# Performance work log

Measured on AMD Instinct MI355X. Metric: run time of the kernel, lower is better.

## Reference

```python
import jax, jax.numpy as jnp
import numpy as np

B, S, E, H = 2, 2048, 768, 12
HD = E // H
EPS = 1e-5


def setup_inputs() -> dict:
    key = jax.random.key(0)
    ks = jax.random.split(key, 7)
    sc_in = 1.0 / np.sqrt(E)
    return {
        "x": jax.random.normal(ks[0], (B, S, E), dtype=jnp.float32),
        "gamma": jnp.ones((E,), dtype=jnp.float32),
        "beta": jnp.zeros((E,), dtype=jnp.float32),
        "Wqkv": jax.random.normal(ks[1], (3 * E, E), dtype=jnp.float32) * sc_in,
        "bqkv": jax.random.normal(ks[2], (3 * E,), dtype=jnp.float32) * 0.01,
        "Wo": jax.random.normal(ks[3], (E, E), dtype=jnp.float32) * sc_in,
        "bo": jax.random.normal(ks[4], (E,), dtype=jnp.float32) * 0.01,
    }


def reference(x, gamma, beta, Wqkv, bqkv, Wo, bo):
    # LayerNorm
    mu = jnp.mean(x, axis=-1, keepdims=True)
    var = jnp.mean(jnp.square(x - mu), axis=-1, keepdims=True)
    xn = (x - mu) * jax.lax.rsqrt(var + EPS) * gamma + beta
    # fused QKV projection; original reshapes to [B,S,H,3*hd] then chunks,
    # i.e. per-head blocks of 3*hd split into q/k/v slices of hd each.
    qkv = (xn @ Wqkv.T + bqkv).reshape(B, S, H, 3, HD)
    q, k, v = qkv[..., 0, :], qkv[..., 1, :], qkv[..., 2, :]  # [B,S,H,hd]
    scores = jnp.einsum("bshd,bthd->bhst", q, k) / np.sqrt(HD)
    attn = jax.nn.softmax(scores, axis=-1)  # [B,H,S,S]
    out = jnp.einsum("bhst,bthd->bshd", attn, v).reshape(B, S, E)
    return out @ Wo.T + bo
```

## Files before the change

kernel.cpp:

```cpp
#include <hip/hip_runtime.h>
#include <math.h>

#define B_  2
#define S_  2048
#define E_  768
#define H_  12
#define HD_ 64
#define M_  (B_ * S_)
#define N3E (3 * E_)

typedef __attribute__((ext_vector_type(8)))  short short8;
typedef __attribute__((ext_vector_type(8)))  _Float16 half8;
typedef __attribute__((ext_vector_type(4)))  _Float16 half4;
typedef __attribute__((ext_vector_type(2)))  _Float16 half2_t;
typedef __attribute__((ext_vector_type(4)))  float floatx4;
typedef __attribute__((ext_vector_type(16))) float floatx16;

#define QSCALE 0.18033688011112042f

__device__ inline unsigned short f2bf(float f) {
  union { float f; unsigned u; } a; a.f = f;
  unsigned r = a.u + 0x7fff + ((a.u >> 16) & 1);
  return (unsigned short)(r >> 16);
}
__device__ inline unsigned short f2bf_fast(float f) {
  union { float f; unsigned u; } a; a.f = f;
  return (unsigned short)((a.u + 0x8000u) >> 16);
}
__device__ inline half2_t pkrtz(float a, float b) {
  return __builtin_bit_cast(half2_t, __builtin_amdgcn_cvt_pkrtz(a, b));
}

__global__ __launch_bounds__(256) void cvt_kernel(
    const float* __restrict__ src, unsigned short* __restrict__ dst, int n4) {
  int i = blockIdx.x * 256 + threadIdx.x;
  if (i < n4) {
    float4 f = *(const float4*)&src[i * 4];
    ushort4 r;
    r.x = f2bf(f.x); r.y = f2bf(f.y); r.z = f2bf(f.z); r.w = f2bf(f.w);
    *(ushort4*)&dst[i * 4] = r;
  }
}

__global__ __launch_bounds__(256) void ln_kernel(
    const float* __restrict__ x, const float* __restrict__ gamma,
    const float* __restrict__ beta, unsigned short* __restrict__ xnb) {
  const int row = blockIdx.x;
  const int t = threadIdx.x;
  const float* xr = x + (size_t)row * E_;

  float v0 = xr[t];
  float v1 = xr[t + 256];
  float v2 = xr[t + 512];
  float s  = v0 + v1 + v2;
  float s2 = v0 * v0 + v1 * v1 + v2 * v2;

  for (int o = 32; o > 0; o >>= 1) {
    s  += __shfl_down(s, o);
    s2 += __shfl_down(s2, o);
  }
  __shared__ float red[8];
  const int wave = t >> 6, lane = t & 63;
  if (lane == 0) { red[wave] = s; red[4 + wave] = s2; }
  __syncthreads();
  s  = red[0] + red[1] + red[2] + red[3];
  s2 = red[4] + red[5] + red[6] + red[7];

  const float mu  = s * (1.0f / E_);
  const float var = s2 * (1.0f / E_) - mu * mu;
  const float rs  = rsqrtf(var + 1e-5f);

  unsigned short* xo = xnb + (size_t)row * E_;
  xo[t]       = f2bf((v0 - mu) * rs * gamma[t]       + beta[t]);
  xo[t + 256] = f2bf((v1 - mu) * rs * gamma[t + 256] + beta[t + 256]);
  xo[t + 512] = f2bf((v2 - mu) * rs * gamma[t + 512] + beta[t + 512]);
}

__global__ __launch_bounds__(256) void bgemm_kernel(
    const unsigned short* __restrict__ A, const unsigned short* __restrict__ Wb,
    const float* __restrict__ bias, int mode,
    unsigned short* __restrict__ qbf, unsigned short* __restrict__ kbf,
    _Float16* __restrict__ vth, float* __restrict__ out) {
  __shared__ __align__(16) unsigned short As[128 * 64];
  __shared__ __align__(16) unsigned short Bs[128 * 64];

  const int t  = threadIdx.x;
  const int ln = t & 63, wv = t >> 6;
  const int lr = ln & 15, lg = ln >> 4;
  const int wr = wv >> 1, wc = wv & 1;
  const int m0 = blockIdx.x * 128, n0 = blockIdx.y * 128;

  const int srow = ln >> 3;
  const int scol = (ln & 7) * 8;

  const unsigned short* Ag = A  + (size_t)(m0 + wv * 32 + srow) * 768 + scol;
  const unsigned short* Bg = Wb + (size_t)(n0 + wv * 32 + srow) * 768 + scol;

  floatx4 acc[4][4];
#pragma unroll
  for (int i = 0; i < 4; i++)
#pragma unroll
    for (int j = 0; j < 4; j++) acc[i][j] = (floatx4){0.f, 0.f, 0.f, 0.f};

  for (int k0 = 0; k0 < 768; k0 += 64) {
    __syncthreads();
#pragma unroll
    for (int j = 0; j < 4; j++) {
      __builtin_amdgcn_global_load_lds(
          (const __attribute__((address_space(1))) void*)(Ag + k0 + j * 8 * 768),
          (__attribute__((address_space(3))) void*)(&As[(wv * 32 + j * 8) * 64]),
          16, 0, 0);
      __builtin_amdgcn_global_load_lds(
          (const __attribute__((address_space(1))) void*)(Bg + k0 + j * 8 * 768),
          (__attribute__((address_space(3))) void*)(&Bs[(wv * 32 + j * 8) * 64]),
          16, 0, 0);
    }
    __syncthreads();

#pragma unroll
    for (int kk = 0; kk < 2; kk++) {
      short8 af[4], bf[4];
#pragma unroll
      for (int i = 0; i < 4; i++)
        af[i] = *(const short8*)&As[(wr * 64 + i * 16 + lr) * 64 + kk * 32 + lg * 8];
#pragma unroll
      for (int j = 0; j < 4; j++)
        bf[j] = *(const short8*)&Bs[(wc * 64 + j * 16 + lr) * 64 + kk * 32 + lg * 8];
#pragma unroll
      for (int i = 0; i < 4; i++)
#pragma unroll
        for (int j = 0; j < 4; j++)
          acc[i][j] = __builtin_amdgcn_mfma_f32_16x16x32_bf16(af[i], bf[j], acc[i][j], 0, 0, 0);
    }
  }

  if (mode == 1) {
#pragma unroll
    for (int i = 0; i < 4; i++) {
      const int grow0 = m0 + wr * 64 + i * 16 + lg * 4;
#pragma unroll
      for (int j = 0; j < 4; j++) {
        const int gcol = n0 + wc * 64 + j * 16 + lr;
        const float bb = bias[gcol];
#pragma unroll
        for (int r = 0; r < 4; r++)
          out[(size_t)(grow0 + r) * E_ + gcol] = acc[i][j][r] + bb;
      }
    }
  } else {
#pragma unroll
    for (int i = 0; i < 4; i++) {
      const int grow0 = m0 + wr * 64 + i * 16 + lg * 4;
      const int bq = grow0 >> 11, s0 = grow0 & 2047;
      const int tb = s0 >> 6, kh = (s0 >> 5) & 1;
#pragma unroll
      for (int j = 0; j < 4; j++) {
        const int n = n0 + wc * 64 + j * 16 + lr;
        const int h = n / 192, w = (n >> 6) % 3, d = n & 63;
        const int bh = bq * H_ + h;
        const float bb = bias[n];
        if (w == 2) {
          const int db = d >> 5, l31v = d & 31;
          const int kc2 = (s0 >> 4) & 1, l5v = (s0 >> 3) & 1, e0 = s0 & 7;
          half2_t h01 = pkrtz(acc[i][j][0] + bb, acc[i][j][1] + bb);
          half2_t h23 = pkrtz(acc[i][j][2] + bb, acc[i][j][3] + bb);
          half4 hv = __builtin_shufflevector(h01, h23, 0, 1, 2, 3);
          const size_t idx =
              ((((((size_t)bh * 32 + tb) * 2 + kh) * 2 + db) * 2 + kc2) * 2 + l5v) * 256
              + (size_t)l31v * 8 + e0;
          *(half4*)&vth[idx] = hv;
        } else {
          unsigned short* dst = (w == 0) ? qbf : kbf;
          const float sc = (w == 0) ? QSCALE : 1.0f;
          const int kc = d >> 4, l5 = (d >> 3) & 1, e = d & 7;
          const size_t basei =
              ((((size_t)bh * 32 + tb) * 2 + kh) * 4 + kc) * 512 + (size_t)l5 * 256 + e;
          const int r0 = (s0 & 31) * 8;
#pragma unroll
          for (int r = 0; r < 4; r++)
            dst[basei + r0 + r * 8] = f2bf_fast((acc[i][j][r] + bb) * sc);
        }
      }
    }
  }
}

#define PROW 40

__global__ __launch_bounds__(256, 4) void attn_kernel(
    const unsigned short* __restrict__ qb, const unsigned short* __restrict__ kb,
    const _Float16* __restrict__ vth, unsigned short* __restrict__ ao) {
  __shared__ __align__(16) unsigned char smem[26112];
  _Float16* Ps = (_Float16*)smem;
  float* C1 = (float*)smem;
  float* C2 = C1 + 3 * 64 * 17;

  const int t = threadIdx.x;
  const int lane = t & 63, wv = t >> 6;
  const int l31 = lane & 31, l5 = lane >> 5;

  const int id = blockIdx.x;
  const int bh = (id & 7) * 3 + ((id >> 3) >> 6);
  const int qt = (id >> 3) & 63;
  const int b = bh / H_, h = bh % H_;
  const int q0 = qt * 32;

  short8 qf[4];
  {
    const unsigned short* qp =
        qb + ((size_t)(bh * 32 + (qt >> 1)) * 2 + (qt & 1)) * 2048 + (size_t)lane * 8;
#pragma unroll
    for (int kc = 0; kc < 4; kc++) qf[kc] = *(const short8*)(qp + kc * 512);
  }
  half8 ones;
#pragma unroll
  for (int i = 0; i < 8; i++) ones[i] = (_Float16)1.0f;

  floatx16 oacc0 = (floatx16)0.0f;
  floatx16 oacc1 = (floatx16)0.0f;
  floatx16 lacc  = (floatx16)0.0f;

  const unsigned short* kpb =
      kb + (size_t)(bh * 32 + (wv >> 1)) * 4096 + (size_t)(wv & 1) * 2048 + (size_t)lane * 8;
  const _Float16* vpb =
      vth + (size_t)(bh * 32 + (wv >> 1)) * 4096 + (size_t)(wv & 1) * 2048 + (size_t)lane * 8;
  _Float16* PsW = Ps + wv * 32 * PROW;

  short8 kf[4];
#pragma unroll
  for (int kc = 0; kc < 4; kc++) kf[kc] = *(const short8*)(kpb + kc * 512);

  for (int tb = 0; tb < 16; tb++) {
    const _Float16* vt = vpb + (size_t)tb * 8192;
    half8 vf0 = *(const half8*)(vt);
    half8 vf1 = *(const half8*)(vt + 512);
    half8 vf2 = *(const half8*)(vt + 1024);
    half8 vf3 = *(const half8*)(vt + 1536);

    floatx16 sacc = (floatx16)0.0f;
#pragma unroll
    for (int kc = 0; kc < 4; kc++)
      sacc = __builtin_amdgcn_mfma_f32_32x32x16_bf16(kf[kc], qf[kc], sacc, 0, 0, 0);

    {
      const unsigned short* kt = kpb + (size_t)((tb + 1) & 15) * 8192;
#pragma unroll
      for (int kc = 0; kc < 4; kc++) kf[kc] = *(const short8*)(kt + kc * 512);
    }

#pragma unroll
    for (int r = 0; r < 16; r++) sacc[r] = exp2f(sacc[r]);
#pragma unroll
    for (int rq = 0; rq < 4; rq++) {
      half2_t a = pkrtz(sacc[rq * 4 + 0], sacc[rq * 4 + 1]);
      half2_t c = pkrtz(sacc[rq * 4 + 2], sacc[rq * 4 + 3]);
      half4 w = __builtin_shufflevector(a, c, 0, 1, 2, 3);
      *(half4*)&PsW[l31 * PROW + rq * 8 + l5 * 4] = w;
    }

    const _Float16* prd = &PsW[l31 * PROW + l5 * 8];
    half8 pf0 = *(const half8*)(prd);
    half8 pf1 = *(const half8*)(prd + 16);

    oacc0 = __builtin_amdgcn_mfma_f32_32x32x16_f16(vf0, pf0, oacc0, 0, 0, 0);
    oacc0 = __builtin_amdgcn_mfma_f32_32x32x16_f16(vf1, pf1, oacc0, 0, 0, 0);
    oacc1 = __builtin_amdgcn_mfma_f32_32x32x16_f16(vf2, pf0, oacc1, 0, 0, 0);
    oacc1 = __builtin_amdgcn_mfma_f32_32x32x16_f16(vf3, pf1, oacc1, 0, 0, 0);
    lacc  = __builtin_amdgcn_mfma_f32_32x32x16_f16(ones, pf0, lacc, 0, 0, 0);
    lacc  = __builtin_amdgcn_mfma_f32_32x32x16_f16(ones, pf1, lacc, 0, 0, 0);
  }

  __syncthreads();
  if (wv > 0) {
    float* c = &C1[(size_t)((wv - 1) * 64 + lane) * 17];
#pragma unroll
    for (int j = 0; j < 16; j++) c[j] = oacc0[j];
    c[16] = lacc[0];
  }
  if (wv != 1) {
    const int slot = (wv == 0) ? 0 : wv - 1;
    float* c = &C2[(size_t)(slot * 64 + lane) * 17];
#pragma unroll
    for (int j = 0; j < 16; j++) c[j] = oacc1[j];
    c[16] = lacc[0];
  }
  __syncthreads();
  if (wv < 2) {
    float o[16];
    float L;
    if (wv == 0) {
      L = lacc[0];
#pragma unroll
      for (int j = 0; j < 16; j++) o[j] = oacc0[j];
#pragma unroll
      for (int i = 0; i < 3; i++) {
        const float* c = &C1[(size_t)(i * 64 + lane) * 17];
#pragma unroll
        for (int j = 0; j < 16; j++) o[j] += c[j];
        L += c[16];
      }
    } else {
      L = lacc[0];
#pragma unroll
      for (int j = 0; j < 16; j++) o[j] = oacc1[j];
#pragma unroll
      for (int i = 0; i < 3; i++) {
        const float* c = &C2[(size_t)(i * 64 + lane) * 17];
#pragma unroll
        for (int j = 0; j < 16; j++) o[j] += c[j];
        L += c[16];
      }
    }
    const float inv = 1.0f / L;
    const int row = q0 + l31;
    const int dbase = wv * 32;
    unsigned short* arow = &ao[((size_t)(b * S_ + row)) * E_ + h * HD_ + dbase];
#pragma unroll
    for (int a = 0; a < 4; a++) {
      ushort4 s;
      s.x = f2bf(o[a * 4 + 0] * inv);
      s.y = f2bf(o[a * 4 + 1] * inv);
      s.z = f2bf(o[a * 4 + 2] * inv);
      s.w = f2bf(o[a * 4 + 3] * inv);
      *(ushort4*)&arow[8 * a + 4 * l5] = s;
    }
  }
}

extern "C" void kernel_launch(void* const* d_in, const int* in_sizes, int n_in,
                              void* d_out, int out_size, void* d_ws, size_t ws_size,
                              hipStream_t stream) {
  const float* x     = (const float*)d_in[0];
  const float* gamma = (const float*)d_in[1];
  const float* beta  = (const float*)d_in[2];
  const float* Wqkv  = (const float*)d_in[3];
  const float* bqkv  = (const float*)d_in[4];
  const float* Wo    = (const float*)d_in[5];
  const float* bo    = (const float*)d_in[6];
  float* out = (float*)d_out;

  const size_t SZ = (size_t)M_ * E_;
  unsigned short* xnb = (unsigned short*)d_ws;
  unsigned short* qbf = xnb + SZ;
  unsigned short* kbf = qbf + SZ;
  _Float16*       vth = (_Float16*)(kbf + SZ);
  unsigned short* aob = (unsigned short*)(vth + SZ);
  unsigned short* wqb = aob + SZ;
  unsigned short* wob = wqb + (size_t)N3E * E_;

  const int nq4 = (N3E * E_) / 4;
  const int no4 = (E_ * E_) / 4;
  cvt_kernel<<<(nq4 + 255) / 256, 256, 0, stream>>>(Wqkv, wqb, nq4);
  cvt_kernel<<<(no4 + 255) / 256, 256, 0, stream>>>(Wo, wob, no4);

  ln_kernel<<<M_, 256, 0, stream>>>(x, gamma, beta, xnb);

  dim3 g_qkv(M_ / 128, N3E / 128);
  bgemm_kernel<<<g_qkv, 256, 0, stream>>>(xnb, wqb, bqkv, 0, qbf, kbf, vth, nullptr);

  attn_kernel<<<1536, 256, 0, stream>>>(qbf, kbf, vth, aob);

  dim3 g_out(M_ / 128, E_ / 128);
  bgemm_kernel<<<g_out, 256, 0, stream>>>(aob, wob, bo, 1, nullptr, nullptr, nullptr, out);
}
```

Baseline: 193.1 us.

## Pipeline attention K/V loads, replace ones-MFMA row sum, merge cvt, vectorize LayerNorm

```diff
diff --git a/kernel.cpp b/kernel.cpp
--- a/kernel.cpp
+++ b/kernel.cpp
@@ -31,49 +31,63 @@
   return __builtin_bit_cast(half2_t, __builtin_amdgcn_cvt_pkrtz(a, b));
 }
 
-__global__ __launch_bounds__(256) void cvt_kernel(
-    const float* __restrict__ src, unsigned short* __restrict__ dst, int n4) {
+__global__ __launch_bounds__(256) void cvt2_kernel(
+    const float* __restrict__ w1, const float* __restrict__ w2,
+    unsigned short* __restrict__ d1, unsigned short* __restrict__ d2,
+    int n1_4, int ntot4) {
   int i = blockIdx.x * 256 + threadIdx.x;
-  if (i < n4) {
-    float4 f = *(const float4*)&src[i * 4];
-    ushort4 r;
-    r.x = f2bf(f.x); r.y = f2bf(f.y); r.z = f2bf(f.z); r.w = f2bf(f.w);
-    *(ushort4*)&dst[i * 4] = r;
-  }
+  if (i >= ntot4) return;
+  const float* src; unsigned short* dst; int k;
+  if (i < n1_4) { src = w1; dst = d1; k = i; }
+  else          { src = w2; dst = d2; k = i - n1_4; }
+  float4 f = *(const float4*)&src[k * 4];
+  ushort4 r;
+  r.x = f2bf(f.x); r.y = f2bf(f.y); r.z = f2bf(f.z); r.w = f2bf(f.w);
+  *(ushort4*)&dst[k * 4] = r;
 }
 
 __global__ __launch_bounds__(256) void ln_kernel(
     const float* __restrict__ x, const float* __restrict__ gamma,
     const float* __restrict__ beta, unsigned short* __restrict__ xnb) {
-  const int row = blockIdx.x;
-  const int t = threadIdx.x;
+  const int wv = threadIdx.x >> 6, lane = threadIdx.x & 63;
+  const int row = blockIdx.x * 4 + wv;
   const float* xr = x + (size_t)row * E_;
 
-  float v0 = xr[t];
-  float v1 = xr[t + 256];
-  float v2 = xr[t + 512];
-  float s  = v0 + v1 + v2;
-  float s2 = v0 * v0 + v1 * v1 + v2 * v2;
-
+  float4 a = ((const float4*)xr)[lane];
+  float4 b = ((const float4*)xr)[lane + 64];
+  float4 c = ((const float4*)xr)[lane + 128];
+
+  float s  = (a.x + a.y) + (a.z + a.w) + (b.x + b.y) + (b.z + b.w)
+           + (c.x + c.y) + (c.z + c.w);
+  float s2 = a.x*a.x + a.y*a.y + a.z*a.z + a.w*a.w
+           + b.x*b.x + b.y*b.y + b.z*b.z + b.w*b.w
+           + c.x*c.x + c.y*c.y + c.z*c.z + c.w*c.w;
+#pragma unroll
   for (int o = 32; o > 0; o >>= 1) {
-    s  += __shfl_down(s, o);
-    s2 += __shfl_down(s2, o);
-  }
-  __shared__ float red[8];
-  const int wave = t >> 6, lane = t & 63;
-  if (lane == 0) { red[wave] = s; red[4 + wave] = s2; }
-  __syncthreads();
-  s  = red[0] + red[1] + red[2] + red[3];
-  s2 = red[4] + red[5] + red[6] + red[7];
-
+    s  += __shfl_xor(s, o);
+    s2 += __shfl_xor(s2, o);
+  }
   const float mu  = s * (1.0f / E_);
   const float var = s2 * (1.0f / E_) - mu * mu;
   const float rs  = rsqrtf(var + 1e-5f);
 
-  unsigned short* xo = xnb + (size_t)row * E_;
-  xo[t]       = f2bf((v0 - mu) * rs * gamma[t]       + beta[t]);
-  xo[t + 256] = f2bf((v1 - mu) * rs * gamma[t + 256] + beta[t + 256]);
-  xo[t + 512] = f2bf((v2 - mu) * rs * gamma[t + 512] + beta[t + 512]);
+  const float4* gp = (const float4*)gamma;
+  const float4* bp = (const float4*)beta;
+  ushort4* xo = (ushort4*)(xnb + (size_t)row * E_);
+
+  float4 vin[3] = {a, b, c};
+#pragma unroll
+  for (int j = 0; j < 3; j++) {
+    float4 g = gp[lane + 64 * j];
+    float4 be = bp[lane + 64 * j];
+    float4 v = vin[j];
+    ushort4 r;
+    r.x = f2bf((v.x - mu) * rs * g.x + be.x);
+    r.y = f2bf((v.y - mu) * rs * g.y + be.y);
+    r.z = f2bf((v.z - mu) * rs * g.z + be.z);
+    r.w = f2bf((v.w - mu) * rs * g.w + be.w);
+    xo[lane + 64 * j] = r;
+  }
 }
 
 __global__ __launch_bounds__(256) void bgemm_kernel(
@@ -212,13 +226,10 @@
 #pragma unroll
     for (int kc = 0; kc < 4; kc++) qf[kc] = *(const short8*)(qp + kc * 512);
   }
-  half8 ones;
-#pragma unroll
-  for (int i = 0; i < 8; i++) ones[i] = (_Float16)1.0f;
 
   floatx16 oacc0 = (floatx16)0.0f;
   floatx16 oacc1 = (floatx16)0.0f;
-  floatx16 lacc  = (floatx16)0.0f;
+  float lsum = 0.f;
 
   const unsigned short* kpb =
       kb + (size_t)(bh * 32 + (wv >> 1)) * 4096 + (size_t)(wv & 1) * 2048 + (size_t)lane * 8;
@@ -227,29 +238,28 @@
   _Float16* PsW = Ps + wv * 32 * PROW;
 
   short8 kf[4];
+  half8 vf[4];
 #pragma unroll
   for (int kc = 0; kc < 4; kc++) kf[kc] = *(const short8*)(kpb + kc * 512);
+  floatx16 sacc = (floatx16)0.0f;
+#pragma unroll
+  for (int kc = 0; kc < 4; kc++)
+    sacc = __builtin_amdgcn_mfma_f32_32x32x16_bf16(kf[kc], qf[kc], sacc, 0, 0, 0);
+#pragma unroll
+  for (int kc = 0; kc < 4; kc++) kf[kc] = *(const short8*)(kpb + 8192 + kc * 512);
+#pragma unroll
+  for (int j = 0; j < 4; j++) vf[j] = *(const half8*)(vpb + j * 512);
 
   for (int tb = 0; tb < 16; tb++) {
-    const _Float16* vt = vpb + (size_t)tb * 8192;
-    half8 vf0 = *(const half8*)(vt);
-    half8 vf1 = *(const half8*)(vt + 512);
-    half8 vf2 = *(const half8*)(vt + 1024);
-    half8 vf3 = *(const half8*)(vt + 1536);
-
-    floatx16 sacc = (floatx16)0.0f;
-#pragma unroll
-    for (int kc = 0; kc < 4; kc++)
-      sacc = __builtin_amdgcn_mfma_f32_32x32x16_bf16(kf[kc], qf[kc], sacc, 0, 0, 0);
-
+#pragma unroll
+    for (int r = 0; r < 16; r++) sacc[r] = exp2f(sacc[r]);
     {
-      const unsigned short* kt = kpb + (size_t)((tb + 1) & 15) * 8192;
-#pragma unroll
-      for (int kc = 0; kc < 4; kc++) kf[kc] = *(const short8*)(kt + kc * 512);
-    }
-
-#pragma unroll
-    for (int r = 0; r < 16; r++) sacc[r] = exp2f(sacc[r]);
+      float s01 = (sacc[0] + sacc[1]) + (sacc[2] + sacc[3]);
+      float s23 = (sacc[4] + sacc[5]) + (sacc[6] + sacc[7]);
+      float s45 = (sacc[8] + sacc[9]) + (sacc[10] + sacc[11]);
+      float s67 = (sacc[12] + sacc[13]) + (sacc[14] + sacc[15]);
+      lsum += (s01 + s23) + (s45 + s67);
+    }
 #pragma unroll
     for (int rq = 0; rq < 4; rq++) {
       half2_t a = pkrtz(sacc[rq * 4 + 0], sacc[rq * 4 + 1]);
@@ -257,39 +267,51 @@
       half4 w = __builtin_shufflevector(a, c, 0, 1, 2, 3);
       *(half4*)&PsW[l31 * PROW + rq * 8 + l5 * 4] = w;
     }
-
     const _Float16* prd = &PsW[l31 * PROW + l5 * 8];
     half8 pf0 = *(const half8*)(prd);
     half8 pf1 = *(const half8*)(prd + 16);
 
-    oacc0 = __builtin_amdgcn_mfma_f32_32x32x16_f16(vf0, pf0, oacc0, 0, 0, 0);
-    oacc0 = __builtin_amdgcn_mfma_f32_32x32x16_f16(vf1, pf1, oacc0, 0, 0, 0);
-    oacc1 = __builtin_amdgcn_mfma_f32_32x32x16_f16(vf2, pf0, oacc1, 0, 0, 0);
-    oacc1 = __builtin_amdgcn_mfma_f32_32x32x16_f16(vf3, pf1, oacc1, 0, 0, 0);
-    lacc  = __builtin_amdgcn_mfma_f32_32x32x16_f16(ones, pf0, lacc, 0, 0, 0);
-    lacc  = __builtin_amdgcn_mfma_f32_32x32x16_f16(ones, pf1, lacc, 0, 0, 0);
-  }
+    oacc0 = __builtin_amdgcn_mfma_f32_32x32x16_f16(vf[0], pf0, oacc0, 0, 0, 0);
+    oacc0 = __builtin_amdgcn_mfma_f32_32x32x16_f16(vf[1], pf1, oacc0, 0, 0, 0);
+    oacc1 = __builtin_amdgcn_mfma_f32_32x32x16_f16(vf[2], pf0, oacc1, 0, 0, 0);
+    oacc1 = __builtin_amdgcn_mfma_f32_32x32x16_f16(vf[3], pf1, oacc1, 0, 0, 0);
+
+    if (tb != 15) {
+      const _Float16* vt2 = vpb + (size_t)(tb + 1) * 8192;
+#pragma unroll
+      for (int j = 0; j < 4; j++) vf[j] = *(const half8*)(vt2 + j * 512);
+      sacc = (floatx16)0.0f;
+#pragma unroll
+      for (int kc = 0; kc < 4; kc++)
+        sacc = __builtin_amdgcn_mfma_f32_32x32x16_bf16(kf[kc], qf[kc], sacc, 0, 0, 0);
+      const unsigned short* kt2 = kpb + (size_t)((tb + 2) & 15) * 8192;
+#pragma unroll
+      for (int kc = 0; kc < 4; kc++) kf[kc] = *(const short8*)(kt2 + kc * 512);
+    }
+  }
+
+  const float l2 = lsum + __shfl_xor(lsum, 32);
 
   __syncthreads();
   if (wv > 0) {
     float* c = &C1[(size_t)((wv - 1) * 64 + lane) * 17];
 #pragma unroll
     for (int j = 0; j < 16; j++) c[j] = oacc0[j];
-    c[16] = lacc[0];
+    c[16] = l2;
   }
   if (wv != 1) {
     const int slot = (wv == 0) ? 0 : wv - 1;
     float* c = &C2[(size_t)(slot * 64 + lane) * 17];
 #pragma unroll
     for (int j = 0; j < 16; j++) c[j] = oacc1[j];
-    c[16] = lacc[0];
+    c[16] = l2;
   }
   __syncthreads();
   if (wv < 2) {
     float o[16];
     float L;
     if (wv == 0) {
-      L = lacc[0];
+      L = l2;
 #pragma unroll
       for (int j = 0; j < 16; j++) o[j] = oacc0[j];
 #pragma unroll
@@ -300,7 +322,7 @@
         L += c[16];
       }
     } else {
-      L = lacc[0];
+      L = l2;
 #pragma unroll
       for (int j = 0; j < 16; j++) o[j] = oacc1[j];
 #pragma unroll
@@ -350,10 +372,10 @@
 
   const int nq4 = (N3E * E_) / 4;
   const int no4 = (E_ * E_) / 4;
-  cvt_kernel<<<(nq4 + 255) / 256, 256, 0, stream>>>(Wqkv, wqb, nq4);
-  cvt_kernel<<<(no4 + 255) / 256, 256, 0, stream>>>(Wo, wob, no4);
-
-  ln_kernel<<<M_, 256, 0, stream>>>(x, gamma, beta, xnb);
+  const int ntot4 = nq4 + no4;
+  cvt2_kernel<<<(ntot4 + 255) / 256, 256, 0, stream>>>(Wqkv, Wo, wqb, wob, nq4, ntot4);
+
+  ln_kernel<<<M_ / 4, 256, 0, stream>>>(x, gamma, beta, xnb);
 
   dim3 g_qkv(M_ / 128, N3E / 128);
   bgemm_kernel<<<g_qkv, 256, 0, stream>>>(xnb, wqb, bqkv, 0, qbf, kbf, vth, nullptr);
```

Result: faster. 182.7 us (-5.4%).
